# Kernel tuning notes

Hardware: AMD Instinct MI355X
Metric: run time of the kernel (lower is better)

## Reference

```python
import jax, jax.numpy as jnp
import numpy as np

B, N = 2, 4096
IN_CH, OUT_CH = 64, 64
L_MAX, NR = 3, 4
KERNEL_RADIUS = 0.5
PATCH = 64  # hardcoded in torch topk(-dist, 64)


def setup_inputs() -> dict:
    key = jax.random.key(0)
    k1, k2, k3 = jax.random.split(key, 3)
    xyz = jax.random.normal(k1, (B, N, 3), dtype=jnp.float32)
    signal = jax.random.normal(k2, (B, N, IN_CH), dtype=jnp.float32)
    # xavier_uniform on (out, in, nr, l_max+1): receptive = nr*(l_max+1)
    recept = NR * (L_MAX + 1)
    bound = float(np.sqrt(6.0 / (IN_CH * recept + OUT_CH * recept)))
    weight = jax.random.uniform(k3, (OUT_CH, IN_CH, NR, L_MAX + 1), dtype=jnp.float32,
                                minval=-bound, maxval=bound)
    biases = jnp.zeros((OUT_CH,), dtype=jnp.float32)
    return {"xyz": xyz, "signal": signal, "weight": weight, "biases": biases}


def _sph(X):
    # X: [B,N,P,3] l2-normalized patch directions -> [B,N,P,(L_MAX+1)^2]
    x, y, z = X[..., 0], X[..., 1], X[..., 2]
    x2, y2, z2 = x * x, y * y, z * z
    Ys = []
    Ys.append(jnp.full_like(x, 0.5 * np.sqrt(1.0 / np.pi)))           # Y00
    s3 = np.sqrt(3.0 / np.pi) / 2.0
    Ys += [s3 * y, s3 * z, -s3 * x]                                    # l=1
    s15h = np.sqrt(15.0 / np.pi) / 2.0
    s15q = np.sqrt(15.0 / np.pi) / 4.0
    s5q = np.sqrt(5.0 / np.pi) / 4.0
    Ys += [s15h * x * y, s15h * y * z, s5q * (2.0 * z2 - x2 - y2),
           -s15h * z * x, s15q * (x2 - y2)]                            # l=2
    c33 = np.sqrt(35.0 / (2.0 * np.pi)) / 4.0
    c32 = np.sqrt(105.0 / np.pi) / 2.0
    c31 = np.sqrt(21.0 / (2.0 * np.pi)) / 4.0
    c30 = np.sqrt(7.0 / np.pi) / 4.0
    c32b = np.sqrt(105.0 / np.pi) / 4.0
    Ys += [c33 * (3.0 * x2 * y - y * y2),
           c32 * x * y * z,
           c31 * (4.0 * y * z2 - x2 * y - y * y2),
           c30 * (2.0 * z * z2 - 3.0 * x2 * z - 3.0 * y2 * z),
           -c31 * (4.0 * z2 * x - x * x2 - x * y2),
           c32b * (x2 * z - y2 * z),
           -c33 * (x * x2 - 3.0 * x * y2)]                             # l=3
    return jnp.stack(Ys, axis=-1)


def reference(xyz, signal, weight, biases):
    # pairwise squared distances via matmul (costly_cdist)
    r2 = jnp.sum(xyz * xyz, axis=2)                                    # [B,N]
    sqd = r2[:, :, None] - 2.0 * jnp.einsum('bnd,bmd->bnm', xyz, xyz) + r2[:, None, :]
    neg_vals, idx = jax.lax.top_k(-sqd, PATCH)                         # KNN
    sq_patches_dist = -neg_vals                                        # [B,N,P]
    gather = jax.vmap(lambda pts, i: pts[i])                           # per-batch fancy gather
    patches = gather(xyz, idx) - xyz[:, :, None, :]                    # [B,N,P,3]
    # F.normalize(p=2, dim=-1, eps=0.01): x / max(||x||, eps)
    nrm = jnp.linalg.norm(patches, axis=-1, keepdims=True)
    Y = _sph(patches / jnp.maximum(nrm, 0.01))                         # [B,N,P,K2]
    dist = jnp.sqrt(jnp.maximum(sq_patches_dist, 1e-4))                # [B,N,P]
    r_grid = jnp.linspace(0.0, KERNEL_RADIUS, NR, dtype=jnp.float32)   # [NR]
    sigma = KERNEL_RADIUS / (NR - 1)
    rad = jnp.exp(-jnp.square(dist[..., None] - r_grid) / (2.0 * sigma ** 2))  # [B,N,P,NR]
    yk = Y[:, :, :, None, :] * rad[..., None]                          # [B,N,P,NR,K2]
    y_w = jnp.sum(yk[:, :, :, 0, 0], axis=2)[:, :, None, None, None]   # [B,N,1,1,1]
    conv_kernel = yk / (y_w + 1e-6)
    sig_patches = gather(signal, idx)                                  # [B,N,P,C]
    y = jnp.einsum('bvprn,bvpc->bvcrn', conv_kernel, sig_patches)
    y = y * y
    bands = [jnp.sum(y[..., l * l:(l + 1) * (l + 1)], axis=-1) for l in range(L_MAX + 1)]
    y = jnp.stack(bands, axis=-1)                                      # [B,N,C,NR,L+1]
    y = jnp.sqrt(jnp.maximum(y, 1e-4))
    out = jnp.einsum('ijrn,bvjrn->bvi', weight, y) + biases
    return out
```

## Files before the change

kernel.cpp:

```cpp
#include <hip/hip_runtime.h>
#include <hip/hip_bf16.h>
#include <math.h>

#define NB 2
#define NPTS 4096
#define CH 64
#define PATCH 64

typedef __attribute__((ext_vector_type(8))) short s16x8;
typedef __attribute__((ext_vector_type(4))) short s16x4;
typedef __attribute__((ext_vector_type(4))) float f32x4;
typedef __attribute__((ext_vector_type(4))) unsigned u32x4;

static __device__ __forceinline__ short f2bf(float f) {
    union { __hip_bfloat16 h; short s; } u;
    u.h = __float2bfloat16(f);
    return u.s;
}

__global__ __launch_bounds__(256) void prep_kernel(const float* __restrict__ W,
                                                   short* __restrict__ Wfrag,
                                                   const float* __restrict__ xyz,
                                                   float4* __restrict__ xyz4) {
    const int bid = blockIdx.x;
    const int tid = threadIdx.x;
    if (bid < 32) {
        const int gid = bid * 256 + tid;
        const int mt = gid >> 11;
        const int st = (gid >> 6) & 31;
        const int l  = gid & 63;
        const int i  = mt * 16 + (l & 15);
        const int k0 = st * 32 + (l >> 4) * 8;
        const f32x4 a = *(const f32x4*)&W[i * 1024 + k0];
        const f32x4 c = *(const f32x4*)&W[i * 1024 + k0 + 4];
        s16x8 v;
        v[0] = f2bf(a[0]); v[1] = f2bf(a[1]); v[2] = f2bf(a[2]); v[3] = f2bf(a[3]);
        v[4] = f2bf(c[0]); v[5] = f2bf(c[1]); v[6] = f2bf(c[2]); v[7] = f2bf(c[3]);
        *(s16x8*)&Wfrag[gid * 8] = v;
    } else {
        const int idx = (bid - 32) * 256 + tid;
        const float x = xyz[idx * 3 + 0];
        const float y = xyz[idx * 3 + 1];
        const float z = xyz[idx * 3 + 2];
        float4 v;
        v.x = x; v.y = y; v.z = z;
        v.w = fmaf(x, x, fmaf(y, y, z * z));
        xyz4[idx] = v;
    }
}

__global__ __launch_bounds__(256, 8) void knn_kernel(const float4* __restrict__ xyz4,
                                                     int* __restrict__ knn_idx) {
    const int pt   = blockIdx.x;
    const int b    = pt >> 12;
    const int q    = pt & (NPTS - 1);
    const int tid  = threadIdx.x;
    const int wv   = tid >> 6;
    const int lane = tid & 63;

    __shared__ __align__(16) unsigned hist[2048];
    __shared__ __align__(16) unsigned short sbin[4096];
    __shared__ unsigned wsum[4];
    __shared__ unsigned sh_H;
    __shared__ int sh_need;
    __shared__ int cnt_less, cnt_tie;

    const float4* xb = xyz4 + (size_t)b * NPTS;
    const float4 qp = xb[q];

#pragma unroll
    for (int u = 0; u < 2; ++u)
        ((u32x4*)hist)[u * 256 + tid] = (u32x4){0u, 0u, 0u, 0u};
    if (tid == 0) { cnt_less = 0; cnt_tie = 0; }
    __syncthreads();

#pragma unroll 4
    for (int i = 0; i < 16; ++i) {
        const int m = i * 256 + tid;
        const float4 p = xb[m];
        const float dx = p.x - qp.x;
        const float dy = p.y - qp.y;
        const float dz = p.z - qp.z;
        const float sq = fmaf(dx, dx, fmaf(dy, dy, dz * dz));
        const unsigned hk = __float_as_uint(sq) >> 19;
        sbin[i * 256 + tid] = (unsigned short)hk;
        atomicAdd(&hist[hk & 2047], 1u << ((hk >> 11) << 4));
    }
    __syncthreads();

    const int wb2 = (tid & 127) * 16;
    const int shp = (tid >> 7) << 4;
    unsigned tsum = 0;
#pragma unroll
    for (int u = 0; u < 4; ++u) {
        const u32x4 h4 = *(const u32x4*)&hist[wb2 + u * 4];
        tsum += ((h4[0] >> shp) & 0xFFFFu) + ((h4[1] >> shp) & 0xFFFFu)
              + ((h4[2] >> shp) & 0xFFFFu) + ((h4[3] >> shp) & 0xFFFFu);
    }
    unsigned run = tsum;
#pragma unroll
    for (int off = 1; off < 64; off <<= 1) {
        const unsigned v = __shfl_up(run, off);
        if (lane >= off) run += v;
    }
    if (lane == 63) wsum[wv] = run;
    __syncthreads();
    unsigned wbase = 0;
    for (int w2 = 0; w2 < wv; ++w2) wbase += wsum[w2];
    const unsigned incl = wbase + run;
    const unsigned excl = incl - tsum;
    if ((int)excl < PATCH && PATCH <= (int)incl) {
        int nrem = PATCH - (int)excl;
        for (int u = 0; u < 16; ++u) {
            const unsigned cb = (hist[wb2 + u] >> shp) & 0xFFFFu;
            if (nrem <= (int)cb) { sh_H = (unsigned)(tid * 16 + u); sh_need = nrem; break; }
            nrem -= (int)cb;
        }
    }
    __syncthreads();

    const unsigned H = sh_H;
    const int need  = sh_need;
    const int nless = PATCH - need;
    int* optr = knn_idx + (size_t)pt * PATCH;
    unsigned* ckey = hist;
    unsigned* cidx = hist + 1024;

#pragma unroll 4
    for (int i = 0; i < 16; ++i) {
        const int m = i * 256 + tid;
        const unsigned hk = sbin[i * 256 + tid];
        if (hk < H) {
            const int pos = atomicAdd(&cnt_less, 1);
            optr[pos] = m;
        } else if (hk == H) {
            const int pos = atomicAdd(&cnt_tie, 1);
            if (pos < 1024) {
                const float4 p = xb[m];
                const float dx = p.x - qp.x;
                const float dy = p.y - qp.y;
                const float dz = p.z - qp.z;
                const float sq = fmaf(dx, dx, fmaf(dy, dy, dz * dz));
                ckey[pos] = __float_as_uint(sq);
                cidx[pos] = m;
            }
        }
    }
    __syncthreads();

    const int nc = min(cnt_tie, 1024);
    for (int i = tid; i < nc; i += 256) {
        const unsigned ki = ckey[i];
        int rank = 0;
        for (int j = 0; j < nc; ++j) {
            const unsigned kj = ckey[j];
            rank += (kj < ki || (kj == ki && j < i)) ? 1 : 0;
        }
        if (rank < need) optr[nless + rank] = cidx[i];
    }
}

__global__ __launch_bounds__(256, 4) void conv_kernel(const float4* __restrict__ xyz4,
                                                      const float* __restrict__ signal,
                                                      const short* __restrict__ Wfrag,
                                                      const float* __restrict__ biases,
                                                      const int* __restrict__ knn_idx,
                                                      float* __restrict__ out) {
    const int tid  = threadIdx.x;
    const int wv   = tid >> 6;
    const int lane = tid & 63;
    const int ln15 = lane & 15;
    const int kq   = lane >> 4;

    __shared__ __align__(16) short cks_bf[4096];
    __shared__ __align__(16) short ckF[4096];
    __shared__ __align__(16) short sigF[4096];
    __shared__ __align__(16) short zb[4 * 1032];
    __shared__ int   sIdx[PATCH];
    __shared__ float sh_inv;

    for (int it = 0; it < 4; ++it) {
        const int pt = blockIdx.x * 4 + it;
        const int b  = pt >> 12;
        const int q  = pt & (NPTS - 1);

        if (tid < PATCH) sIdx[tid] = knn_idx[(size_t)pt * PATCH + tid];
        __syncthreads();

        if (wv == 0) {
            const int p   = lane;
            const int idx = sIdx[p];
            const float4 cp = xyz4[(size_t)b * NPTS + q];
            const float4 np = xyz4[(size_t)b * NPTS + idx];
            const float dx = np.x - cp.x;
            const float dy = np.y - cp.y;
            const float dz = np.z - cp.z;
            const float nrm2 = dx * dx + dy * dy + dz * dz;
            const float inv_n = 1.0f / fmaxf(sqrtf(nrm2), 0.01f);
            const float x = dx * inv_n, y = dy * inv_n, z = dz * inv_n;
            const float x2 = x * x, y2 = y * y, zz = z * z;

            float Y[16];
            Y[0] = 0.28209479177387814f;
            const float s3 = 0.4886025119029199f;
            Y[1] = s3 * y;  Y[2] = s3 * z;  Y[3] = -s3 * x;
            const float s15h = 1.0925484305920792f;
            const float s15q = 0.5462742152960396f;
            const float s5q  = 0.31539156525252005f;
            Y[4] = s15h * x * y;
            Y[5] = s15h * y * z;
            Y[6] = s5q * (2.0f * zz - x2 - y2);
            Y[7] = -s15h * z * x;
            Y[8] = s15q * (x2 - y2);
            const float c33  = 0.5900435899266435f;
            const float c32  = 2.8906114426405543f;
            const float c31  = 0.4570457994644658f;
            const float c30  = 0.3731763325901154f;
            const float c32b = 1.4453057213202771f;
            Y[9]  = c33 * (3.0f * x2 * y - y * y2);
            Y[10] = c32 * x * y * z;
            Y[11] = c31 * (4.0f * y * zz - x2 * y - y * y2);
            Y[12] = c30 * (2.0f * z * zz - 3.0f * x2 * z - 3.0f * y2 * z);
            Y[13] = -c31 * (4.0f * zz * x - x * x2 - x * y2);
            Y[14] = c32b * (x2 * z - y2 * z);
            Y[15] = -c33 * (x * x2 - 3.0f * x * y2);

            const float dist = sqrtf(fmaxf(nrm2, 1e-4f));
            const float d1 = dist - 0.16666667f;
            const float d2 = dist - 0.33333334f;
            const float d3 = dist - 0.5f;
            float rad[4];
            rad[0] = expf(-dist * dist * 18.0f);
            rad[1] = expf(-d1 * d1 * 18.0f);
            rad[2] = expf(-d2 * d2 * 18.0f);
            rad[3] = expf(-d3 * d3 * 18.0f);

            const int pm = p & 15;
#pragma unroll
            for (int chunk = 0; chunk < 16; ++chunk) {
                const int r  = chunk >> 2;
                const int kb = (chunk & 3) * 4;
                s16x4 v;
                v[0] = f2bf(Y[kb + 0] * rad[r]);
                v[1] = f2bf(Y[kb + 1] * rad[r]);
                v[2] = f2bf(Y[kb + 2] * rad[r]);
                v[3] = f2bf(Y[kb + 3] * rad[r]);
                *(s16x4*)&cks_bf[p * 64 + ((chunk ^ pm) << 2)] = v;
            }
            float v = 0.28209479177387814f * rad[0];
#pragma unroll
            for (int off = 32; off > 0; off >>= 1) v += __shfl_down(v, off);
            if (p == 0) sh_inv = 1.0f / (v + 1e-6f);
        } else {
            const int r0 = (wv - 1) * 3;
            const int rn = (wv == 3) ? 2 : 3;
            for (int rr = 0; rr < rn; ++rr) {
                const int rd = r0 + rr;
                const int ct = rd >> 1, s = rd & 1;
                const int c  = ct * 16 + ln15;
                const int pb = s * 32 + kq * 8;
                s16x8 sv;
#pragma unroll
                for (int j = 0; j < 8; ++j) {
                    const float f = signal[(size_t)(b * NPTS + sIdx[pb + j]) * CH + c];
                    sv[j] = f2bf(f);
                }
                *(s16x8*)&sigF[(ct * 2 + s) * 512 + lane * 8] = sv;
            }
        }
        __syncthreads();

#pragma unroll
        for (int ff = 0; ff < 2; ++ff) {
            const int f  = wv + ff * 4;
            const int mt = f >> 1, s = f & 1;
            const int rk = mt * 16 + ln15;
            const int rsw = rk >> 2, rlo = rk & 3;
            const int pb = s * 32 + kq * 8;
            s16x8 av;
#pragma unroll
            for (int j = 0; j < 8; ++j) {
                const int p = pb + j;
                av[j] = cks_bf[p * 64 + ((rsw ^ (p & 15)) << 2) + rlo];
            }
            *(s16x8*)&ckF[f * 512 + lane * 8] = av;
        }
        __syncthreads();

        const s16x8 bf0 = *(const s16x8*)&sigF[(wv * 2 + 0) * 512 + lane * 8];
        const s16x8 bf1 = *(const s16x8*)&sigF[(wv * 2 + 1) * 512 + lane * 8];
        f32x4 acc0 = {0.f, 0.f, 0.f, 0.f}, acc1 = acc0, acc2 = acc0, acc3 = acc0;
        {
            s16x8 a;
            a = *(const s16x8*)&ckF[0 * 512 + lane * 8];
            acc0 = __builtin_amdgcn_mfma_f32_16x16x32_bf16(a, bf0, acc0, 0, 0, 0);
            a = *(const s16x8*)&ckF[1 * 512 + lane * 8];
            acc0 = __builtin_amdgcn_mfma_f32_16x16x32_bf16(a, bf1, acc0, 0, 0, 0);
            a = *(const s16x8*)&ckF[2 * 512 + lane * 8];
            acc1 = __builtin_amdgcn_mfma_f32_16x16x32_bf16(a, bf0, acc1, 0, 0, 0);
            a = *(const s16x8*)&ckF[3 * 512 + lane * 8];
            acc1 = __builtin_amdgcn_mfma_f32_16x16x32_bf16(a, bf1, acc1, 0, 0, 0);
            a = *(const s16x8*)&ckF[4 * 512 + lane * 8];
            acc2 = __builtin_amdgcn_mfma_f32_16x16x32_bf16(a, bf0, acc2, 0, 0, 0);
            a = *(const s16x8*)&ckF[5 * 512 + lane * 8];
            acc2 = __builtin_amdgcn_mfma_f32_16x16x32_bf16(a, bf1, acc2, 0, 0, 0);
            a = *(const s16x8*)&ckF[6 * 512 + lane * 8];
            acc3 = __builtin_amdgcn_mfma_f32_16x16x32_bf16(a, bf0, acc3, 0, 0, 0);
            a = *(const s16x8*)&ckF[7 * 512 + lane * 8];
            acc3 = __builtin_amdgcn_mfma_f32_16x16x32_bf16(a, bf1, acc3, 0, 0, 0);
        }

        const float inv = sh_inv;
        const int qq = kq;
        float rb[4][4];
#pragma unroll
        for (int mt = 0; mt < 4; ++mt) {
            f32x4 av = (mt == 0) ? acc0 : (mt == 1) ? acc1 : (mt == 2) ? acc2 : acc3;
            const float y0 = av[0] * inv, y1 = av[1] * inv;
            const float y2 = av[2] * inv, y3 = av[3] * inv;
            const float sA = y0 * y0;
            const float sB = y1 * y1 + y2 * y2 + y3 * y3;
            const float sAll = sA + sB;
            float b0 = (qq == 0) ? sA : 0.0f;
            float b1 = (qq == 0) ? sB : 0.0f;
            float b2 = (qq == 1) ? sAll : ((qq == 2) ? sA : 0.0f);
            float b3 = (qq == 3) ? sAll : ((qq == 2) ? sB : 0.0f);
            b0 += __shfl_xor(b0, 16); b0 += __shfl_xor(b0, 32);
            b1 += __shfl_xor(b1, 16); b1 += __shfl_xor(b1, 32);
            b2 += __shfl_xor(b2, 16); b2 += __shfl_xor(b2, 32);
            b3 += __shfl_xor(b3, 16); b3 += __shfl_xor(b3, 32);
            rb[mt][0] = b0; rb[mt][1] = b1; rb[mt][2] = b2; rb[mt][3] = b3;
        }
        float s0 = rb[0][0], s1 = rb[0][1], s2 = rb[0][2], s3 = rb[0][3];
#pragma unroll
        for (int mt = 1; mt < 4; ++mt) {
            s0 = (qq == mt) ? rb[mt][0] : s0;
            s1 = (qq == mt) ? rb[mt][1] : s1;
            s2 = (qq == mt) ? rb[mt][2] : s2;
            s3 = (qq == mt) ? rb[mt][3] : s3;
        }
        s16x4 zv;
        zv[0] = f2bf(sqrtf(fmaxf(s0, 1e-4f)));
        zv[1] = f2bf(sqrtf(fmaxf(s1, 1e-4f)));
        zv[2] = f2bf(sqrtf(fmaxf(s2, 1e-4f)));
        zv[3] = f2bf(sqrtf(fmaxf(s3, 1e-4f)));
        const int c = wv * 16 + ln15;
        *(s16x4*)&zb[it * 1032 + c * 16 + qq * 4] = zv;
    }
    __syncthreads();

    const int mt5 = wv;
    const int g   = ln15 & 3;
    f32x4 acc5 = {0.f, 0.f, 0.f, 0.f};
#pragma unroll 4
    for (int st = 0; st < 32; ++st) {
        const s16x8 a  = *(const s16x8*)&Wfrag[((mt5 * 32 + st) * 64 + lane) * 8];
        const s16x8 zf = *(const s16x8*)&zb[g * 1032 + st * 32 + kq * 8];
        acc5 = __builtin_amdgcn_mfma_f32_16x16x32_bf16(a, zf, acc5, 0, 0, 0);
    }
    if (ln15 < 4) {
        const int i0 = mt5 * 16 + kq * 4;
        const int orow = (blockIdx.x * 4 + g) * CH;
#pragma unroll
        for (int rg = 0; rg < 4; ++rg)
            out[orow + i0 + rg] = acc5[rg] + biases[i0 + rg];
    }
}

extern "C" void kernel_launch(void* const* d_in, const int* in_sizes, int n_in,
                              void* d_out, int out_size, void* d_ws, size_t ws_size,
                              hipStream_t stream) {
    const float* xyz    = (const float*)d_in[0];
    const float* signal = (const float*)d_in[1];
    const float* weight = (const float*)d_in[2];
    const float* biases = (const float*)d_in[3];
    float* out = (float*)d_out;

    char* ws = (char*)d_ws;
    int*    knn_idx = (int*)ws;
    short*  Wfrag   = (short*)(ws + (size_t)NB * NPTS * PATCH * sizeof(int));
    float4* xyz4    = (float4*)(ws + (size_t)NB * NPTS * PATCH * sizeof(int) + 131072);

    prep_kernel<<<64, 256, 0, stream>>>(weight, Wfrag, xyz, xyz4);
    knn_kernel<<<NB * NPTS, 256, 0, stream>>>(xyz4, knn_idx);
    conv_kernel<<<(NB * NPTS) / 4, 256, 0, stream>>>(xyz4, signal, Wfrag, biases,
                                                     knn_idx, out);
}
```

Before: 87.18 us.

## Pre-convert signal to bf16 and prefetch next point's gathers in conv kernel

Adds a prep stage that converts the signal to bf16 once, halving the bytes gathered per neighbor. The conv kernel now loads all four points' knn indices up front and prefetches the next iteration's neighbor coordinates and signal rows into registers while the current MFMA stage runs. The signal gather is spread over two waves instead of three. This adds register pressure and an extra barrier per iteration, and the prep kernel now does more work.

New measurement: 88.19 us. No clear change (+1.2%).

```diff
diff --git a/kernel.cpp b/kernel.cpp
--- a/kernel.cpp
+++ b/kernel.cpp
@@ -21,7 +21,9 @@
 __global__ __launch_bounds__(256) void prep_kernel(const float* __restrict__ W,
                                                    short* __restrict__ Wfrag,
                                                    const float* __restrict__ xyz,
-                                                   float4* __restrict__ xyz4) {
+                                                   float4* __restrict__ xyz4,
+                                                   const float* __restrict__ signal,
+                                                   unsigned short* __restrict__ sigbf) {
     const int bid = blockIdx.x;
     const int tid = threadIdx.x;
     if (bid < 32) {
@@ -37,7 +39,7 @@
         v[0] = f2bf(a[0]); v[1] = f2bf(a[1]); v[2] = f2bf(a[2]); v[3] = f2bf(a[3]);
         v[4] = f2bf(c[0]); v[5] = f2bf(c[1]); v[6] = f2bf(c[2]); v[7] = f2bf(c[3]);
         *(s16x8*)&Wfrag[gid * 8] = v;
-    } else {
+    } else if (bid < 64) {
         const int idx = (bid - 32) * 256 + tid;
         const float x = xyz[idx * 3 + 0];
         const float y = xyz[idx * 3 + 1];
@@ -46,6 +48,16 @@
         v.x = x; v.y = y; v.z = z;
         v.w = fmaf(x, x, fmaf(y, y, z * z));
         xyz4[idx] = v;
+    } else {
+        const int g = (bid - 64) * 256 + tid;
+        const size_t base = (size_t)g * 32;
+#pragma unroll
+        for (int u = 0; u < 8; ++u) {
+            const f32x4 v = *(const f32x4*)&signal[base + u * 4];
+            s16x4 o;
+            o[0] = f2bf(v[0]); o[1] = f2bf(v[1]); o[2] = f2bf(v[2]); o[3] = f2bf(v[3]);
+            *(s16x4*)&sigbf[base + u * 4] = o;
+        }
     }
 }
 
@@ -161,7 +173,7 @@
 }
 
 __global__ __launch_bounds__(256, 4) void conv_kernel(const float4* __restrict__ xyz4,
-                                                      const float* __restrict__ signal,
+                                                      const unsigned short* __restrict__ sigbf,
                                                       const short* __restrict__ Wfrag,
                                                       const float* __restrict__ biases,
                                                       const int* __restrict__ knn_idx,
@@ -176,25 +188,42 @@
     __shared__ __align__(16) short ckF[4096];
     __shared__ __align__(16) short sigF[4096];
     __shared__ __align__(16) short zb[4 * 1032];
-    __shared__ int   sIdx[PATCH];
+    __shared__ int   sIdx4[256];
     __shared__ float sh_inv;
 
+    sIdx4[tid] = knn_idx[(size_t)blockIdx.x * 256 + tid];
+    __syncthreads();
+
+    const int b = blockIdx.x >> 10;
+    const float4* xbase = xyz4 + (size_t)b * NPTS;
+    const unsigned short* sgb = sigbf + (size_t)b * NPTS * CH;
+
+    float4 pcp, pnp;
+    s16x8 pre0, pre1, pre2, pre3;
+
+    if (wv == 0) {
+        pcp = xbase[(blockIdx.x * 4) & (NPTS - 1)];
+        pnp = xbase[sIdx4[lane]];
+    } else if (wv <= 2) {
+        const int s  = wv - 1;
+        const int pb = s * 32 + kq * 8;
+#pragma unroll
+        for (int j = 0; j < 8; ++j) {
+            const int row = sIdx4[pb + j];
+            const unsigned short* rp = sgb + ((size_t)row << 6) + ln15;
+            pre0[j] = (short)rp[0];
+            pre1[j] = (short)rp[16];
+            pre2[j] = (short)rp[32];
+            pre3[j] = (short)rp[48];
+        }
+    }
+
     for (int it = 0; it < 4; ++it) {
-        const int pt = blockIdx.x * 4 + it;
-        const int b  = pt >> 12;
-        const int q  = pt & (NPTS - 1);
-
-        if (tid < PATCH) sIdx[tid] = knn_idx[(size_t)pt * PATCH + tid];
-        __syncthreads();
-
         if (wv == 0) {
-            const int p   = lane;
-            const int idx = sIdx[p];
-            const float4 cp = xyz4[(size_t)b * NPTS + q];
-            const float4 np = xyz4[(size_t)b * NPTS + idx];
-            const float dx = np.x - cp.x;
-            const float dy = np.y - cp.y;
-            const float dz = np.z - cp.z;
+            const int p = lane;
+            const float dx = pnp.x - pcp.x;
+            const float dy = pnp.y - pcp.y;
+            const float dz = pnp.z - pcp.z;
             const float nrm2 = dx * dx + dy * dy + dz * dz;
             const float inv_n = 1.0f / fmaxf(sqrtf(nrm2), 0.01f);
             const float x = dx * inv_n, y = dy * inv_n, z = dz * inv_n;
@@ -251,22 +280,12 @@
 #pragma unroll
             for (int off = 32; off > 0; off >>= 1) v += __shfl_down(v, off);
             if (p == 0) sh_inv = 1.0f / (v + 1e-6f);
-        } else {
-            const int r0 = (wv - 1) * 3;
-            const int rn = (wv == 3) ? 2 : 3;
-            for (int rr = 0; rr < rn; ++rr) {
-                const int rd = r0 + rr;
-                const int ct = rd >> 1, s = rd & 1;
-                const int c  = ct * 16 + ln15;
-                const int pb = s * 32 + kq * 8;
-                s16x8 sv;
-#pragma unroll
-                for (int j = 0; j < 8; ++j) {
-                    const float f = signal[(size_t)(b * NPTS + sIdx[pb + j]) * CH + c];
-                    sv[j] = f2bf(f);
-                }
-                *(s16x8*)&sigF[(ct * 2 + s) * 512 + lane * 8] = sv;
-            }
+        } else if (wv <= 2) {
+            const int s = wv - 1;
+            *(s16x8*)&sigF[(0 * 2 + s) * 512 + lane * 8] = pre0;
+            *(s16x8*)&sigF[(1 * 2 + s) * 512 + lane * 8] = pre1;
+            *(s16x8*)&sigF[(2 * 2 + s) * 512 + lane * 8] = pre2;
+            *(s16x8*)&sigF[(3 * 2 + s) * 512 + lane * 8] = pre3;
         }
         __syncthreads();
 
@@ -286,6 +305,25 @@
             *(s16x8*)&ckF[f * 512 + lane * 8] = av;
         }
         __syncthreads();
+
+        if (it < 3) {
+            if (wv == 0) {
+                pcp = xbase[(blockIdx.x * 4 + it + 1) & (NPTS - 1)];
+                pnp = xbase[sIdx4[(it + 1) * 64 + lane]];
+            } else if (wv <= 2) {
+                const int s  = wv - 1;
+                const int pb = s * 32 + kq * 8;
+#pragma unroll
+                for (int j = 0; j < 8; ++j) {
+                    const int row = sIdx4[(it + 1) * 64 + pb + j];
+                    const unsigned short* rp = sgb + ((size_t)row << 6) + ln15;
+                    pre0[j] = (short)rp[0];
+                    pre1[j] = (short)rp[16];
+                    pre2[j] = (short)rp[32];
+                    pre3[j] = (short)rp[48];
+                }
+            }
+        }
 
         const s16x8 bf0 = *(const s16x8*)&sigF[(wv * 2 + 0) * 512 + lane * 8];
         const s16x8 bf1 = *(const s16x8*)&sigF[(wv * 2 + 1) * 512 + lane * 8];
@@ -346,6 +384,8 @@
         zv[3] = f2bf(sqrtf(fmaxf(s3, 1e-4f)));
         const int c = wv * 16 + ln15;
         *(s16x4*)&zb[it * 1032 + c * 16 + qq * 4] = zv;
+
+        if (it < 3) __syncthreads();
     }
     __syncthreads();
 
@@ -377,12 +417,13 @@
     float* out = (float*)d_out;
 
     char* ws = (char*)d_ws;
-    int*    knn_idx = (int*)ws;
-    short*  Wfrag   = (short*)(ws + (size_t)NB * NPTS * PATCH * sizeof(int));
-    float4* xyz4    = (float4*)(ws + (size_t)NB * NPTS * PATCH * sizeof(int) + 131072);
-
-    prep_kernel<<<64, 256, 0, stream>>>(weight, Wfrag, xyz, xyz4);
+    int*            knn_idx = (int*)ws;
+    short*          Wfrag   = (short*)(ws + 0x200000);
+    float4*         xyz4    = (float4*)(ws + 0x220000);
+    unsigned short* sigbf   = (unsigned short*)(ws + 0x240000);
+
+    prep_kernel<<<128, 256, 0, stream>>>(weight, Wfrag, xyz, xyz4, signal, sigbf);
     knn_kernel<<<NB * NPTS, 256, 0, stream>>>(xyz4, knn_idx);
-    conv_kernel<<<(NB * NPTS) / 4, 256, 0, stream>>>(xyz4, signal, Wfrag, biases,
+    conv_kernel<<<(NB * NPTS) / 4, 256, 0, stream>>>(xyz4, sigbf, Wfrag, biases,
                                                      knn_idx, out);
 }
```
